# Performance work log

Measured on AMD Instinct MI355X. Metric: run time of the kernel, lower is better.

Reference implementation:

```python
import jax, jax.numpy as jnp
import numpy as np
from jax.scipy.special import logsumexp

TEMPERATURE = 0.1
EPS = 1e-8  # matches torch F.cosine_similarity eps


def setup_inputs() -> dict:
    key = jax.random.key(0)
    k1, k2 = jax.random.split(key)
    N, D, NUM_CLASSES = 8192, 256, 64
    embeddings = jax.random.normal(k1, (N, D), dtype=jnp.float32)
    target = jax.random.randint(k2, (N,), 0, NUM_CLASSES, dtype=jnp.int64)
    return {"embeddings": embeddings, "target": target}


def reference(embeddings, target):
    N = target.shape[0]
    # cosine similarity: normalize rows, then a single GEMM for all pairs
    norms = jnp.linalg.norm(embeddings, axis=-1, keepdims=True)
    e = embeddings / jnp.maximum(norms, EPS)
    sim = (e @ e.T) / TEMPERATURE  # [N, N]

    pos = target[:, None] == target[None, :]  # [N, N] bool, incl. diagonal
    diag = jnp.eye(N, dtype=bool)
    neg_inf = jnp.asarray(-jnp.inf, dtype=sim.dtype)

    # denominator: negatives only (positives masked to -inf)
    lse_neg = logsumexp(jnp.where(pos, neg_inf, sim), axis=1)
    # numerator: positives excluding self (diagonal masked to -inf)
    lse_pos = logsumexp(jnp.where(pos & ~diag, sim, neg_inf), axis=1)

    loss = lse_neg - lse_pos
    return loss.sum()
```

## Files before the change

kernel.cpp:

```cpp
#include <hip/hip_runtime.h>
#include <hip/hip_bf16.h>
#include <stdint.h>

#define NROWS 8192
#define DIM   256
#define BJ    256
#define BI    128
#define KCB   128
#define NKC   2
#define NJT   (NROWS/BJ)
#define NIT   (NROWS/BI)

typedef __attribute__((ext_vector_type(4))) int   int4v;
typedef __attribute__((ext_vector_type(8))) int   int8v;
typedef __attribute__((ext_vector_type(4))) float floatx4;

typedef const __attribute__((address_space(1))) uint32_t gas_u32;
typedef __attribute__((address_space(3))) uint32_t las_u32;

#define SCALE_1_16 0x7B7B7B7B

__device__ __forceinline__ void gload_lds16(const void* g, void* l) {
    __builtin_amdgcn_global_load_lds((gas_u32*)(uintptr_t)g,
                                     (las_u32*)(uintptr_t)l, 16, 0, 0);
}

__global__ __launch_bounds__(256) void normalize_kernel(const float* __restrict__ emb,
                                                        uint32_t* __restrict__ e8)
{
    int row  = blockIdx.x * 4 + (threadIdx.x >> 6);
    int lane = threadIdx.x & 63;
    const float4* rowp = (const float4*)(emb + (size_t)row * DIM);
    float4 v = rowp[lane];
    float ss = v.x*v.x + v.y*v.y + v.z*v.z + v.w*v.w;
    #pragma unroll
    for (int off = 32; off > 0; off >>= 1)
        ss += __shfl_xor(ss, off, 64);
    float inv = 16.0f / fmaxf(sqrtf(ss), 1e-8f);
    int r = __builtin_amdgcn_cvt_pk_fp8_f32(v.x * inv, v.y * inv, 0, false);
    r     = __builtin_amdgcn_cvt_pk_fp8_f32(v.z * inv, v.w * inv, r, true);
    e8[(size_t)row * (DIM / 4) + lane] = (uint32_t)r;
}

__global__ __launch_bounds__(256, 2) void tile_kernel(const uint8_t* __restrict__ e8,
                                                      const int* __restrict__ tgt,
                                                      float* __restrict__ ppos,
                                                      float* __restrict__ pneg)
{
    __shared__ uint8_t sA[BJ * KCB];
    __shared__ uint8_t sB[BI * KCB];
    __shared__ float rsp[2][BI];
    __shared__ float rsn[2][BI];
    __shared__ int   sTi[BI];
    __shared__ int   sTj[BJ];

    const int bi   = blockIdx.x;
    const int bj   = blockIdx.y;
    const int tid  = threadIdx.x;
    const int wave = tid >> 6;
    const int lane = tid & 63;
    const int quad = lane >> 4;
    const int m    = lane & 15;

    if (tid < BI) sTi[tid] = tgt[bi * BI + tid];
    sTj[tid] = tgt[bj * BJ + tid];

    floatx4 acc[8][4];
    #pragma unroll
    for (int a = 0; a < 8; ++a)
        #pragma unroll
        for (int b = 0; b < 4; ++b)
            acc[a][b] = (floatx4){0.f, 0.f, 0.f, 0.f};

    const int wr = (wave >> 1) * 128;
    const int wc = (wave & 1) * 64;

    int goffA[8];
    #pragma unroll
    for (int t = 0; t < 8; ++t) {
        int s   = wave * 512 + t * 64 + lane;
        int row = s >> 3;
        int lc  = (s & 7) ^ (row & 7);
        goffA[t] = row * 256 + lc * 16;
    }
    int goffB[4];
    #pragma unroll
    for (int t = 0; t < 4; ++t) {
        int s   = wave * 256 + t * 64 + lane;
        int row = s >> 3;
        int lc  = (s & 7) ^ (row & 7);
        goffB[t] = row * 256 + lc * 16;
    }

    const char* gA = (const char*)(e8 + (size_t)bj * BJ * 256);
    const char* gB = (const char*)(e8 + (size_t)bi * BI * 256);

    const int xr = m & 7;
    const int c0 = (((quad << 1)    ) ^ xr) << 4;
    const int c1 = (((quad << 1) | 1) ^ xr) << 4;

    for (int kc = 0; kc < NKC; ++kc) {
        #pragma unroll
        for (int t = 0; t < 8; ++t)
            gload_lds16(gA + goffA[t] + kc * KCB, sA + wave * 8192 + t * 1024);
        #pragma unroll
        for (int t = 0; t < 4; ++t)
            gload_lds16(gB + goffB[t] + kc * KCB, sB + wave * 4096 + t * 1024);
        __syncthreads();

        int8v bfr[4];
        #pragma unroll
        for (int tc = 0; tc < 4; ++tc) {
            const uint8_t* pb = sB + (wc + tc * 16 + m) * KCB;
            int4v lo = *(const int4v*)(pb + c0);
            int4v hi = *(const int4v*)(pb + c1);
            bfr[tc] = __builtin_shufflevector(lo, hi, 0, 1, 2, 3, 4, 5, 6, 7);
        }
        #pragma unroll
        for (int tj = 0; tj < 8; ++tj) {
            const uint8_t* pa = sA + (wr + tj * 16 + m) * KCB;
            int4v lo = *(const int4v*)(pa + c0);
            int4v hi = *(const int4v*)(pa + c1);
            int8v af = __builtin_shufflevector(lo, hi, 0, 1, 2, 3, 4, 5, 6, 7);
            #pragma unroll
            for (int tc = 0; tc < 4; ++tc)
                acc[tj][tc] = __builtin_amdgcn_mfma_scale_f32_16x16x128_f8f6f4(
                    af, bfr[tc], acc[tj][tc], 0, 0,
                    0, SCALE_1_16, 0, SCALE_1_16);
        }
        __syncthreads();
    }

    int ti4[4];
    #pragma unroll
    for (int tc = 0; tc < 4; ++tc) ti4[tc] = sTi[wc + tc * 16 + m];

    float ps[4] = {0.f, 0.f, 0.f, 0.f};
    float ns[4] = {0.f, 0.f, 0.f, 0.f};

    #pragma unroll
    for (int tj = 0; tj < 8; ++tj) {
        const int jl = wr + tj * 16 + (quad << 2);
        const int jglob = bj * BJ + jl;
        int tjv[4];
        #pragma unroll
        for (int r = 0; r < 4; ++r) tjv[r] = sTj[jl + r];
        #pragma unroll
        for (int tc = 0; tc < 4; ++tc) {
            const int iglob = bi * BI + wc + tc * 16 + m;
            const int tiv = ti4[tc];
            #pragma unroll
            for (int r = 0; r < 4; ++r) {
                float v = __expf(fmaf(10.f, acc[tj][tc][r], -10.f));
                if (jglob + r == iglob) v = 0.f;
                const bool pos = (tjv[r] == tiv);
                ps[tc] += pos ? v : 0.f;
                ns[tc] += pos ? 0.f : v;
            }
        }
    }

    #pragma unroll
    for (int tc = 0; tc < 4; ++tc) {
        ps[tc] += __shfl_xor(ps[tc], 16, 64);
        ps[tc] += __shfl_xor(ps[tc], 32, 64);
        ns[tc] += __shfl_xor(ns[tc], 16, 64);
        ns[tc] += __shfl_xor(ns[tc], 32, 64);
    }
    if (quad == 0) {
        #pragma unroll
        for (int tc = 0; tc < 4; ++tc) {
            rsp[wave >> 1][wc + tc * 16 + m] = ps[tc];
            rsn[wave >> 1][wc + tc * 16 + m] = ns[tc];
        }
    }
    __syncthreads();

    if (tid < BI) {
        size_t idx = (size_t)bj * NROWS + (size_t)bi * BI + tid;
        ppos[idx] = rsp[0][tid] + rsp[1][tid];
        pneg[idx] = rsn[0][tid] + rsn[1][tid];
    }
}

__global__ __launch_bounds__(256) void finalize_kernel(const float* __restrict__ ppos,
                                                       const float* __restrict__ pneg,
                                                       float* __restrict__ out)
{
    const int i = blockIdx.x * 256 + threadIdx.x;
    float sp = 0.f, sn = 0.f;
    #pragma unroll 8
    for (int jt = 0; jt < NJT; ++jt) {
        sp += ppos[(size_t)jt * NROWS + i];
        sn += pneg[(size_t)jt * NROWS + i];
    }
    float loss = logf(sn) - logf(sp);
    #pragma unroll
    for (int off = 32; off > 0; off >>= 1)
        loss += __shfl_xor(loss, off, 64);
    __shared__ float w4[4];
    if ((threadIdx.x & 63) == 0) w4[threadIdx.x >> 6] = loss;
    __syncthreads();
    if (threadIdx.x == 0)
        atomicAdd(out, w4[0] + w4[1] + w4[2] + w4[3]);
}

extern "C" void kernel_launch(void* const* d_in, const int* in_sizes, int n_in,
                              void* d_out, int out_size, void* d_ws, size_t ws_size,
                              hipStream_t stream)
{
    (void)in_sizes; (void)n_in; (void)out_size; (void)ws_size;
    const float* emb = (const float*)d_in[0];
    const int*   tgt = (const int*)d_in[1];
    float*       out = (float*)d_out;

    uint32_t* e8   = (uint32_t*)d_ws;
    float*    ppos = (float*)((char*)d_ws + (size_t)NROWS * 256);
    float*    pneg = ppos + (size_t)NJT * NROWS;

    hipMemsetAsync(d_out, 0, sizeof(float), stream);

    normalize_kernel<<<NROWS / 4, 256, 0, stream>>>(emb, e8);

    dim3 grid(NIT, NJT);
    tile_kernel<<<grid, 256, 0, stream>>>((const uint8_t*)e8, tgt, ppos, pneg);

    finalize_kernel<<<NROWS / 256, 256, 0, stream>>>(ppos, pneg, out);
}
```

Before: 99.48 us.

## Load MFMA fragments directly from global, drop LDS staging and block syncs

The tile kernel no longer stages A/B tiles through shared memory with global_load_lds and barriers. Each lane loads its fp8 MFMA fragments straight from global/L2, and target labels come from global instead of LDS. The epilogue now accumulates a total sum plus a positive sum (negatives are recovered as total minus positive in finalize), the diagonal mask is applied only for diagonal tiles, and per-wave partials are written directly, which doubles the partial buffers finalize reads. This trades LDS traffic and syncs for redundant global loads, and the total-minus-positive subtraction may cost some precision.

```diff
diff --git a/kernel.cpp b/kernel.cpp
--- a/kernel.cpp
+++ b/kernel.cpp
@@ -1,13 +1,12 @@
 #include <hip/hip_runtime.h>
 #include <hip/hip_bf16.h>
 #include <stdint.h>
+#include <math.h>
 
 #define NROWS 8192
 #define DIM   256
 #define BJ    256
 #define BI    128
-#define KCB   128
-#define NKC   2
 #define NJT   (NROWS/BJ)
 #define NIT   (NROWS/BI)
 
@@ -15,15 +14,8 @@
 typedef __attribute__((ext_vector_type(8))) int   int8v;
 typedef __attribute__((ext_vector_type(4))) float floatx4;
 
-typedef const __attribute__((address_space(1))) uint32_t gas_u32;
-typedef __attribute__((address_space(3))) uint32_t las_u32;
-
 #define SCALE_1_16 0x7B7B7B7B
-
-__device__ __forceinline__ void gload_lds16(const void* g, void* l) {
-    __builtin_amdgcn_global_load_lds((gas_u32*)(uintptr_t)g,
-                                     (las_u32*)(uintptr_t)l, 16, 0, 0);
-}
+#define L2E10      14.4269504088896f
 
 __global__ __launch_bounds__(256) void normalize_kernel(const float* __restrict__ emb,
                                                         uint32_t* __restrict__ e8)
@@ -42,18 +34,40 @@
     e8[(size_t)row * (DIM / 4) + lane] = (uint32_t)r;
 }
 
+template<bool DIAG>
+__device__ __forceinline__ void epilogue_accum(const floatx4 acc[8][4],
+                                               const int* __restrict__ tgt,
+                                               int bi, int bj, int wr, int wc,
+                                               int quad, int m,
+                                               const int tiv[4], const int ic[4],
+                                               float ps[4], float ts[4])
+{
+    const int jb = bj * BJ + wr + (quad << 2);
+    #pragma unroll
+    for (int tj = 0; tj < 8; ++tj) {
+        const int jg = jb + tj * 16;
+        const int4v t4 = *(const int4v*)(tgt + jg);
+        #pragma unroll
+        for (int tc = 0; tc < 4; ++tc) {
+            const int tivc = tiv[tc];
+            #pragma unroll
+            for (int r = 0; r < 4; ++r) {
+                float v = exp2f(fmaf(L2E10, acc[tj][tc][r], -L2E10));
+                if (DIAG) {
+                    if (jg + r == ic[tc]) v = 0.f;
+                }
+                ts[tc] += v;
+                ps[tc] += (t4[r] == tivc) ? v : 0.f;
+            }
+        }
+    }
+}
+
 __global__ __launch_bounds__(256, 2) void tile_kernel(const uint8_t* __restrict__ e8,
                                                       const int* __restrict__ tgt,
-                                                      float* __restrict__ ppos,
-                                                      float* __restrict__ pneg)
+                                                      float* __restrict__ pps,
+                                                      float* __restrict__ pts)
 {
-    __shared__ uint8_t sA[BJ * KCB];
-    __shared__ uint8_t sB[BI * KCB];
-    __shared__ float rsp[2][BI];
-    __shared__ float rsn[2][BI];
-    __shared__ int   sTi[BI];
-    __shared__ int   sTj[BJ];
-
     const int bi   = blockIdx.x;
     const int bj   = blockIdx.y;
     const int tid  = threadIdx.x;
@@ -62,8 +76,8 @@
     const int quad = lane >> 4;
     const int m    = lane & 15;
 
-    if (tid < BI) sTi[tid] = tgt[bi * BI + tid];
-    sTj[tid] = tgt[bj * BJ + tid];
+    const int wr = (wave >> 1) * 128;
+    const int wc = (wave & 1) * 64;
 
     floatx4 acc[8][4];
     #pragma unroll
@@ -72,129 +86,74 @@
         for (int b = 0; b < 4; ++b)
             acc[a][b] = (floatx4){0.f, 0.f, 0.f, 0.f};
 
-    const int wr = (wave >> 1) * 128;
-    const int wc = (wave & 1) * 64;
+    const uint8_t* pA = e8 + (size_t)(bj * BJ + wr + m) * 256 + quad * 32;
+    const uint8_t* pB = e8 + (size_t)(bi * BI + wc + m) * 256 + quad * 32;
 
-    int goffA[8];
     #pragma unroll
-    for (int t = 0; t < 8; ++t) {
-        int s   = wave * 512 + t * 64 + lane;
-        int row = s >> 3;
-        int lc  = (s & 7) ^ (row & 7);
-        goffA[t] = row * 256 + lc * 16;
-    }
-    int goffB[4];
-    #pragma unroll
-    for (int t = 0; t < 4; ++t) {
-        int s   = wave * 256 + t * 64 + lane;
-        int row = s >> 3;
-        int lc  = (s & 7) ^ (row & 7);
-        goffB[t] = row * 256 + lc * 16;
-    }
-
-    const char* gA = (const char*)(e8 + (size_t)bj * BJ * 256);
-    const char* gB = (const char*)(e8 + (size_t)bi * BI * 256);
-
-    const int xr = m & 7;
-    const int c0 = (((quad << 1)    ) ^ xr) << 4;
-    const int c1 = (((quad << 1) | 1) ^ xr) << 4;
-
-    for (int kc = 0; kc < NKC; ++kc) {
-        #pragma unroll
-        for (int t = 0; t < 8; ++t)
-            gload_lds16(gA + goffA[t] + kc * KCB, sA + wave * 8192 + t * 1024);
-        #pragma unroll
-        for (int t = 0; t < 4; ++t)
-            gload_lds16(gB + goffB[t] + kc * KCB, sB + wave * 4096 + t * 1024);
-        __syncthreads();
-
+    for (int kc = 0; kc < 2; ++kc) {
         int8v bfr[4];
         #pragma unroll
-        for (int tc = 0; tc < 4; ++tc) {
-            const uint8_t* pb = sB + (wc + tc * 16 + m) * KCB;
-            int4v lo = *(const int4v*)(pb + c0);
-            int4v hi = *(const int4v*)(pb + c1);
-            bfr[tc] = __builtin_shufflevector(lo, hi, 0, 1, 2, 3, 4, 5, 6, 7);
-        }
+        for (int tc = 0; tc < 4; ++tc)
+            bfr[tc] = *(const int8v*)(pB + tc * 16 * 256 + kc * 128);
+        int8v af[8];
         #pragma unroll
-        for (int tj = 0; tj < 8; ++tj) {
-            const uint8_t* pa = sA + (wr + tj * 16 + m) * KCB;
-            int4v lo = *(const int4v*)(pa + c0);
-            int4v hi = *(const int4v*)(pa + c1);
-            int8v af = __builtin_shufflevector(lo, hi, 0, 1, 2, 3, 4, 5, 6, 7);
+        for (int tj = 0; tj < 8; ++tj)
+            af[tj] = *(const int8v*)(pA + tj * 16 * 256 + kc * 128);
+
+        #pragma unroll
+        for (int tj = 0; tj < 8; ++tj)
             #pragma unroll
             for (int tc = 0; tc < 4; ++tc)
                 acc[tj][tc] = __builtin_amdgcn_mfma_scale_f32_16x16x128_f8f6f4(
-                    af, bfr[tc], acc[tj][tc], 0, 0,
+                    af[tj], bfr[tc], acc[tj][tc], 0, 0,
                     0, SCALE_1_16, 0, SCALE_1_16);
-        }
-        __syncthreads();
     }
 
-    int ti4[4];
+    int tiv[4], ic[4];
     #pragma unroll
-    for (int tc = 0; tc < 4; ++tc) ti4[tc] = sTi[wc + tc * 16 + m];
+    for (int tc = 0; tc < 4; ++tc) {
+        ic[tc]  = bi * BI + wc + tc * 16 + m;
+        tiv[tc] = tgt[ic[tc]];
+    }
 
     float ps[4] = {0.f, 0.f, 0.f, 0.f};
-    float ns[4] = {0.f, 0.f, 0.f, 0.f};
+    float ts[4] = {0.f, 0.f, 0.f, 0.f};
 
-    #pragma unroll
-    for (int tj = 0; tj < 8; ++tj) {
-        const int jl = wr + tj * 16 + (quad << 2);
-        const int jglob = bj * BJ + jl;
-        int tjv[4];
-        #pragma unroll
-        for (int r = 0; r < 4; ++r) tjv[r] = sTj[jl + r];
-        #pragma unroll
-        for (int tc = 0; tc < 4; ++tc) {
-            const int iglob = bi * BI + wc + tc * 16 + m;
-            const int tiv = ti4[tc];
-            #pragma unroll
-            for (int r = 0; r < 4; ++r) {
-                float v = __expf(fmaf(10.f, acc[tj][tc][r], -10.f));
-                if (jglob + r == iglob) v = 0.f;
-                const bool pos = (tjv[r] == tiv);
-                ps[tc] += pos ? v : 0.f;
-                ns[tc] += pos ? 0.f : v;
-            }
-        }
-    }
+    if ((bi >> 1) == bj)
+        epilogue_accum<true >(acc, tgt, bi, bj, wr, wc, quad, m, tiv, ic, ps, ts);
+    else
+        epilogue_accum<false>(acc, tgt, bi, bj, wr, wc, quad, m, tiv, ic, ps, ts);
 
     #pragma unroll
     for (int tc = 0; tc < 4; ++tc) {
         ps[tc] += __shfl_xor(ps[tc], 16, 64);
         ps[tc] += __shfl_xor(ps[tc], 32, 64);
-        ns[tc] += __shfl_xor(ns[tc], 16, 64);
-        ns[tc] += __shfl_xor(ns[tc], 32, 64);
+        ts[tc] += __shfl_xor(ts[tc], 16, 64);
+        ts[tc] += __shfl_xor(ts[tc], 32, 64);
     }
     if (quad == 0) {
+        const size_t base = (size_t)(bj * 2 + (wave >> 1)) * NROWS;
         #pragma unroll
         for (int tc = 0; tc < 4; ++tc) {
-            rsp[wave >> 1][wc + tc * 16 + m] = ps[tc];
-            rsn[wave >> 1][wc + tc * 16 + m] = ns[tc];
+            pps[base + ic[tc]] = ps[tc];
+            pts[base + ic[tc]] = ts[tc];
         }
-    }
-    __syncthreads();
-
-    if (tid < BI) {
-        size_t idx = (size_t)bj * NROWS + (size_t)bi * BI + tid;
-        ppos[idx] = rsp[0][tid] + rsp[1][tid];
-        pneg[idx] = rsn[0][tid] + rsn[1][tid];
     }
 }
 
-__global__ __launch_bounds__(256) void finalize_kernel(const float* __restrict__ ppos,
-                                                       const float* __restrict__ pneg,
+__global__ __launch_bounds__(256) void finalize_kernel(const float* __restrict__ pps,
+                                                       const float* __restrict__ pts,
                                                        float* __restrict__ out)
 {
     const int i = blockIdx.x * 256 + threadIdx.x;
-    float sp = 0.f, sn = 0.f;
+    float sp = 0.f, st = 0.f;
     #pragma unroll 8
-    for (int jt = 0; jt < NJT; ++jt) {
-        sp += ppos[(size_t)jt * NROWS + i];
-        sn += pneg[(size_t)jt * NROWS + i];
+    for (int t = 0; t < NJT * 2; ++t) {
+        sp += pps[(size_t)t * NROWS + i];
+        st += pts[(size_t)t * NROWS + i];
     }
-    float loss = logf(sn) - logf(sp);
+    float ns = st - sp;
+    float loss = logf(ns) - logf(sp);
     #pragma unroll
     for (int off = 32; off > 0; off >>= 1)
         loss += __shfl_xor(loss, off, 64);
@@ -214,16 +173,16 @@
     const int*   tgt = (const int*)d_in[1];
     float*       out = (float*)d_out;
 
-    uint32_t* e8   = (uint32_t*)d_ws;
-    float*    ppos = (float*)((char*)d_ws + (size_t)NROWS * 256);
-    float*    pneg = ppos + (size_t)NJT * NROWS;
+    uint32_t* e8  = (uint32_t*)d_ws;
+    float*    pps = (float*)((char*)d_ws + (size_t)NROWS * 256);
+    float*    pts = pps + (size_t)NJT * 2 * NROWS;
 
     hipMemsetAsync(d_out, 0, sizeof(float), stream);
 
     normalize_kernel<<<NROWS / 4, 256, 0, stream>>>(emb, e8);
 
     dim3 grid(NIT, NJT);
-    tile_kernel<<<grid, 256, 0, stream>>>((const uint8_t*)e8, tgt, ppos, pneg);
+    tile_kernel<<<grid, 256, 0, stream>>>((const uint8_t*)e8, tgt, pps, pts);
 
-    finalize_kernel<<<NROWS / 256, 256, 0, stream>>>(ppos, pneg, out);
+    finalize_kernel<<<NROWS / 256, 256, 0, stream>>>(pps, pts, out);
 }
```

Result: slower. 130.2 us (+30.9%).
